# Optimization experiments

Hardware: AMD Instinct MI355X
Metric: run time of the kernel (lower is better)

## Reference

```python
import jax, jax.numpy as jnp
import numpy as np

D_MODEL = 512
NUM_HEADS = 8
D_K = D_MODEL // NUM_HEADS


def setup_inputs() -> dict:
    key = jax.random.key(0)
    k0, k1, k2, k3, k4 = jax.random.split(key, 5)
    s = 1.0 / np.sqrt(D_MODEL)
    return {
        "x": jax.random.normal(k0, (2, 4096, D_MODEL), dtype=jnp.float32),
        "W_q": jax.random.normal(k1, (D_MODEL, D_MODEL), dtype=jnp.float32) * s,
        "W_k": jax.random.normal(k2, (D_MODEL, D_MODEL), dtype=jnp.float32) * s,
        "W_v": jax.random.normal(k3, (D_MODEL, D_MODEL), dtype=jnp.float32) * s,
        "W_o": jax.random.normal(k4, (D_MODEL, D_MODEL), dtype=jnp.float32) * s,
    }


def reference(x, W_q, W_k, W_v, W_o):
    B, S, _ = x.shape
    # project and split heads: (B, H, S, d_k)
    def split(t):
        return t.reshape(B, S, NUM_HEADS, D_K).transpose(0, 2, 1, 3)
    Q = split(x @ W_q)
    K = split(x @ W_k)
    V = split(x @ W_v)
    scale = jnp.sqrt(jnp.asarray(D_K, dtype=x.dtype))
    logits = jnp.einsum('bhqd,bhkd->bhqk', Q, K) / scale
    attn = jax.nn.softmax(logits, axis=-1)  # dropout is identity at inference
    out = jnp.einsum('bhqk,bhkd->bhqd', attn, V)
    concat = out.transpose(0, 2, 1, 3).reshape(B, S, D_MODEL)
    return concat @ W_o
```

## Files before the change

### kernel.cpp

```cpp
#include <hip/hip_runtime.h>
#include <hip/hip_bf16.h>


#define DMODEL 512
#define SEQ    4096
#define NTOK   8192
#define LDQK   1024

using f32x4 = __attribute__((ext_vector_type(4))) float;
using s16x8 = __attribute__((ext_vector_type(8))) short;
using u16x8 = __attribute__((ext_vector_type(8))) unsigned short;

static __device__ __forceinline__ unsigned short f2bf(float f) {
  union { float f; unsigned u; } v; v.f = f;
  unsigned r = v.u + 0x7fff + ((v.u >> 16) & 1);
  return (unsigned short)(r >> 16);
}

static __device__ __forceinline__ unsigned pack_bf2(float lo, float hi) {
  __hip_bfloat162 t = __float22bfloat162_rn(make_float2(lo, hi));
  union { __hip_bfloat162 b; unsigned u; } c; c.b = t; return c.u;
}

static __device__ __forceinline__ void gll16(const void* g, void* l) {
  __builtin_amdgcn_global_load_lds(
      (const __attribute__((address_space(1))) unsigned int*)g,
      (__attribute__((address_space(3))) unsigned int*)l, 16, 0, 0);
}

__global__ void prep_kernel(const float* __restrict__ x,
                            const float* __restrict__ Wq,
                            const float* __restrict__ Wk,
                            const float* __restrict__ Wv,
                            const float* __restrict__ Wo,
                            unsigned short* __restrict__ xb,
                            unsigned short* __restrict__ Wall, float c2) {
  __shared__ float T[64][65];
  const int bx = blockIdx.x;
  if (bx < 1024) {
    for (int i = bx * 256 + threadIdx.x; i < NTOK * DMODEL / 4; i += 262144) {
      float4 v = ((const float4*)x)[i];
      ushort4 o;
      o.x = f2bf(v.x); o.y = f2bf(v.y); o.z = f2bf(v.z); o.w = f2bf(v.w);
      ((ushort4*)xb)[i] = o;
    }
    return;
  }
  const int t = bx - 1024;
  const int y = t >> 6, sub = t & 63;
  const float* W = (y == 0) ? Wq : (y == 1) ? Wk : (y == 2) ? Wv : Wo;
  const float scale = (y == 0) ? c2 : 1.0f;
  const int tk = (sub & 7) * 64;
  const int tn = (sub >> 3) * 64;
  const int r  = threadIdx.x >> 2;
  const int cq = threadIdx.x & 3;
#pragma unroll
  for (int i = 0; i < 4; ++i) {
    int c = (cq + 4 * i) * 4;
    float4 v = *(const float4*)&W[(size_t)(tk + r) * 512 + tn + c];
    T[r][c + 0] = v.x * scale; T[r][c + 1] = v.y * scale;
    T[r][c + 2] = v.z * scale; T[r][c + 3] = v.w * scale;
  }
  __syncthreads();
  const int n  = threadIdx.x >> 2;
  const int k0 = (threadIdx.x & 3) * 16;
#pragma unroll
  for (int j4 = 0; j4 < 4; ++j4) {
    ushort4 o;
    o.x = f2bf(T[k0 + j4 * 4 + 0][n]);
    o.y = f2bf(T[k0 + j4 * 4 + 1][n]);
    o.z = f2bf(T[k0 + j4 * 4 + 2][n]);
    o.w = f2bf(T[k0 + j4 * 4 + 3][n]);
    *(ushort4*)&Wall[(size_t)y * 262144 + (size_t)(tn + n) * 512 + tk + k0 + j4 * 4] = o;
  }
}

__global__ __launch_bounds__(256, 3) void gemm_qkv(
    const unsigned short* __restrict__ xb,
    const unsigned short* __restrict__ Wall,
    unsigned short* __restrict__ QKb,
    unsigned short* __restrict__ Vtb)
{
  __shared__ unsigned short As[128 * 64];
  __shared__ unsigned short Bs[128 * 64];
  const int by = blockIdx.y;
  const bool vmode = (by >= 8);
  const unsigned short* A  = vmode ? (Wall + 2 * 262144) : xb;
  const unsigned short* Bt = vmode ? xb : Wall;
  const size_t bm = vmode ? (size_t)(by - 8) * 128 : (size_t)blockIdx.x * 128;
  const size_t bn = vmode ? (size_t)blockIdx.x * 128 : (size_t)by * 128;
  const int tid  = threadIdx.x;
  const int wave = tid >> 6, lane = tid & 63;
  const int q4 = lane >> 4, ln = lane & 15;
  const int wm = (wave >> 1) * 64, wn = (wave & 1) * 64;
  f32x4 acc[4][4] = {};

  const int rlo  = lane >> 3;
  const int sbx  = ((lane & 7) << 4) ^ (rlo << 4);
  const int rswz = (ln & 7) << 4;

  const char* Asb = (const char*)A  + (size_t)(bm + wave * 32 + rlo) * 1024 + sbx;
  const char* Bsb = (const char*)Bt + (size_t)(bn + wave * 32 + rlo) * 1024 + sbx;
  char* Adst = (char*)As + wave * 4096;
  char* Bdst = (char*)Bs + wave * 4096;

  for (int kt = 0; kt < 512; kt += 64) {
    __syncthreads();
#pragma unroll
    for (int j = 0; j < 4; ++j) {
      gll16(Asb + kt * 2 + j * 8192, Adst + j * 1024);
      gll16(Bsb + kt * 2 + j * 8192, Bdst + j * 1024);
    }
    __syncthreads();
    s16x8 bfr[4][2];
#pragma unroll
    for (int ni = 0; ni < 4; ni++) {
      const char* bb = (char*)Bs + (wn + ni * 16 + ln) * 128;
      bfr[ni][0] = *(const s16x8*)(bb + ((q4 * 16)      ^ rswz));
      bfr[ni][1] = *(const s16x8*)(bb + ((q4 * 16 + 64) ^ rswz));
    }
#pragma unroll
    for (int mi = 0; mi < 4; mi++) {
      const char* ab = (char*)As + (wm + mi * 16 + ln) * 128;
      s16x8 af0 = *(const s16x8*)(ab + ((q4 * 16)      ^ rswz));
      s16x8 af1 = *(const s16x8*)(ab + ((q4 * 16 + 64) ^ rswz));
#pragma unroll
      for (int ni = 0; ni < 4; ni++) {
        acc[mi][ni] = __builtin_amdgcn_mfma_f32_16x16x32_bf16(
            af0, bfr[ni][0], acc[mi][ni], 0, 0, 0);
        acc[mi][ni] = __builtin_amdgcn_mfma_f32_16x16x32_bf16(
            af1, bfr[ni][1], acc[mi][ni], 0, 0, 0);
      }
    }
  }
#pragma unroll
  for (int mi = 0; mi < 4; mi++)
#pragma unroll
    for (int r = 0; r < 4; ++r) {
      size_t row = bm + wm + mi * 16 + q4 * 4 + r;
#pragma unroll
      for (int ni = 0; ni < 4; ni++) {
        size_t col = bn + wn + ni * 16 + ln;
        unsigned short hv = f2bf(acc[mi][ni][r]);
        if (!vmode) {
          QKb[row * 1024 + col] = hv;
        } else {
          int b = (int)(col >> 12), s = (int)(col & 4095);
          int sp = (s & ~63) | (s & 32) | (((s >> 2) & 3) << 3) |
                   (((s >> 4) & 1) << 2) | (s & 3);
          Vtb[(size_t)b * 2097152 + row * 4096 + sp] = hv;
        }
      }
    }
}

__global__ __launch_bounds__(256, 2) void attn_kernel(
    const unsigned short* __restrict__ QK,
    const unsigned short* __restrict__ Vt,
    unsigned short* __restrict__ Oc)
{
  const int bid = blockIdx.x + 32 * (blockIdx.y + 8 * blockIdx.z);
  const int lin = (bid & 7) * 64 + (bid >> 3);
  const int qt = lin & 31, bh = lin >> 5;
  const int h = bh & 7, b = bh >> 3;
  const int tid = threadIdx.x, wave = tid >> 6, lane = tid & 63;
  const int q4 = lane >> 4, ln = lane & 15;
  __shared__ unsigned short Ks[2][64 * 64];
  __shared__ unsigned short Vs[2][64 * 64];
  const size_t rowbase = (size_t)b * SEQ;
  const size_t qrow0   = (size_t)qt * 128 + wave * 32;
  const unsigned short* Kp  = QK + rowbase * LDQK + 512 + h * 64;
  const unsigned short* VTp = Vt + ((size_t)(b * 8 + h) * 64) * SEQ;

  s16x8 qf[2][2];
#pragma unroll
  for (int mf = 0; mf < 2; ++mf) {
    const unsigned short* q = QK + (rowbase + qrow0 + mf * 16 + ln) * LDQK + h * 64;
    qf[mf][0] = *(const s16x8*)(q + q4 * 8);
    qf[mf][1] = *(const s16x8*)(q + 32 + q4 * 8);
  }
  f32x4 o[2][4] = {};
  float lp[2] = {};

  const int srow = tid >> 2;
  const int c32  = (tid & 3) * 32;
  const int swz  = (srow & 7) << 4;
  const int wof0 = srow * 128 + ((c32 +  0) ^ swz);
  const int wof1 = srow * 128 + ((c32 + 16) ^ swz);
  const int rswz = (ln & 7) << 4;

  const unsigned short* kgp = Kp  + (size_t)srow * LDQK + (c32 >> 1);
  const unsigned short* vgp = VTp + (size_t)srow * SEQ + (c32 >> 1);

  u16x8 kr  = *(const u16x8*)kgp;
  u16x8 kr2 = *(const u16x8*)(kgp + 8);
  u16x8 vr  = *(const u16x8*)vgp;
  u16x8 vr2 = *(const u16x8*)(vgp + 8);
  *(u16x8*)((char*)Ks[0] + wof0) = kr;
  *(u16x8*)((char*)Ks[0] + wof1) = kr2;
  *(u16x8*)((char*)Vs[0] + wof0) = vr;
  *(u16x8*)((char*)Vs[0] + wof1) = vr2;
  kgp += (size_t)64 * LDQK;  vgp += 64;
  kr  = *(const u16x8*)kgp;
  kr2 = *(const u16x8*)(kgp + 8);
  vr  = *(const u16x8*)vgp;
  vr2 = *(const u16x8*)(vgp + 8);
  __syncthreads();

  const f32x4 fz = {0.f, 0.f, 0.f, 0.f};

  s16x8 vfp[2][4];
  s16x8 pfp[2][2];

  {
    const char* Kc = (const char*)Ks[0];
    const char* Vc = (const char*)Vs[0];
    f32x4 s4[2][4];
#pragma unroll
    for (int ni = 0; ni < 4; ni++) {
      const char* kb = Kc + (ni * 16 + ln) * 128;
      s16x8 kf0 = *(const s16x8*)(kb + ((q4 * 16)      ^ rswz));
      s16x8 kf1 = *(const s16x8*)(kb + ((q4 * 16 + 64) ^ rswz));
      __builtin_amdgcn_s_setprio(1);
#pragma unroll
      for (int mf = 0; mf < 2; ++mf) {
        f32x4 acc0 = __builtin_amdgcn_mfma_f32_16x16x32_bf16(kf0, qf[mf][0], fz, 0, 0, 0);
        s4[mf][ni] = __builtin_amdgcn_mfma_f32_16x16x32_bf16(kf1, qf[mf][1], acc0, 0, 0, 0);
      }
      __builtin_amdgcn_s_setprio(0);
    }
#pragma unroll
    for (int ks = 0; ks < 2; ++ks)
#pragma unroll
      for (int ni = 0; ni < 4; ni++)
        vfp[ks][ni] = *(const s16x8*)(Vc + (ni * 16 + ln) * 128 +
                                      ((ks * 64 + q4 * 16) ^ rswz));
#pragma unroll
    for (int mf = 0; mf < 2; ++mf) {
      float e[4][4];
#pragma unroll
      for (int ni = 0; ni < 4; ni++)
#pragma unroll
        for (int r = 0; r < 4; ++r)
          e[ni][r] = __builtin_amdgcn_exp2f(s4[mf][ni][r]);
      float t0 = (e[0][0] + e[0][1]) + (e[0][2] + e[0][3]);
      float t1 = (e[1][0] + e[1][1]) + (e[1][2] + e[1][3]);
      float t2 = (e[2][0] + e[2][1]) + (e[2][2] + e[2][3]);
      float t3 = (e[3][0] + e[3][1]) + (e[3][2] + e[3][3]);
      lp[mf] += (t0 + t1) + (t2 + t3);
#pragma unroll
      for (int ks = 0; ks < 2; ++ks) {
        union { s16x8 v; unsigned u[4]; } pu;
        pu.u[0] = pack_bf2(e[2 * ks][0],     e[2 * ks][1]);
        pu.u[1] = pack_bf2(e[2 * ks][2],     e[2 * ks][3]);
        pu.u[2] = pack_bf2(e[2 * ks + 1][0], e[2 * ks + 1][1]);
        pu.u[3] = pack_bf2(e[2 * ks + 1][2], e[2 * ks + 1][3]);
        pfp[mf][ks] = pu.v;
      }
    }
    char* Kn = (char*)Ks[1];
    char* Vn = (char*)Vs[1];
    *(u16x8*)(Kn + wof0) = kr;
    *(u16x8*)(Kn + wof1) = kr2;
    *(u16x8*)(Vn + wof0) = vr;
    *(u16x8*)(Vn + wof1) = vr2;
    kgp += (size_t)64 * LDQK;  vgp += 64;
    kr  = *(const u16x8*)kgp;
    kr2 = *(const u16x8*)(kgp + 8);
    vr  = *(const u16x8*)vgp;
    vr2 = *(const u16x8*)(vgp + 8);
    __syncthreads();
  }

#pragma unroll 2
  for (int t = 1; t < 64; ++t) {
    const int cur = t & 1;
    const char* Kc = (const char*)Ks[cur];
    const char* Vc = (const char*)Vs[cur];

    f32x4 s4[2][4];
#pragma unroll
    for (int ni = 0; ni < 4; ni++) {
      const char* kb = Kc + (ni * 16 + ln) * 128;
      s16x8 kf0 = *(const s16x8*)(kb + ((q4 * 16)      ^ rswz));
      s16x8 kf1 = *(const s16x8*)(kb + ((q4 * 16 + 64) ^ rswz));
      __builtin_amdgcn_s_setprio(1);
#pragma unroll
      for (int mf = 0; mf < 2; ++mf) {
        f32x4 acc0 = __builtin_amdgcn_mfma_f32_16x16x32_bf16(kf0, qf[mf][0], fz, 0, 0, 0);
        s4[mf][ni] = __builtin_amdgcn_mfma_f32_16x16x32_bf16(kf1, qf[mf][1], acc0, 0, 0, 0);
      }
      __builtin_amdgcn_s_setprio(0);
    }

#pragma unroll
    for (int ks = 0; ks < 2; ++ks)
#pragma unroll
      for (int ni = 0; ni < 4; ni++)
#pragma unroll
        for (int mf = 0; mf < 2; ++mf)
          o[mf][ni] = __builtin_amdgcn_mfma_f32_16x16x32_bf16(pfp[mf][ks], vfp[ks][ni], o[mf][ni], 0, 0, 0);

    s16x8 vfc[2][4];
#pragma unroll
    for (int ks = 0; ks < 2; ++ks)
#pragma unroll
      for (int ni = 0; ni < 4; ni++)
        vfc[ks][ni] = *(const s16x8*)(Vc + (ni * 16 + ln) * 128 +
                                      ((ks * 64 + q4 * 16) ^ rswz));

    s16x8 pfc[2][2];
#pragma unroll
    for (int mf = 0; mf < 2; ++mf) {
      float e[4][4];
#pragma unroll
      for (int ni = 0; ni < 4; ni++)
#pragma unroll
        for (int r = 0; r < 4; ++r)
          e[ni][r] = __builtin_amdgcn_exp2f(s4[mf][ni][r]);
      float t0 = (e[0][0] + e[0][1]) + (e[0][2] + e[0][3]);
      float t1 = (e[1][0] + e[1][1]) + (e[1][2] + e[1][3]);
      float t2 = (e[2][0] + e[2][1]) + (e[2][2] + e[2][3]);
      float t3 = (e[3][0] + e[3][1]) + (e[3][2] + e[3][3]);
      lp[mf] += (t0 + t1) + (t2 + t3);
#pragma unroll
      for (int ks = 0; ks < 2; ++ks) {
        union { s16x8 v; unsigned u[4]; } pu;
        pu.u[0] = pack_bf2(e[2 * ks][0],     e[2 * ks][1]);
        pu.u[1] = pack_bf2(e[2 * ks][2],     e[2 * ks][3]);
        pu.u[2] = pack_bf2(e[2 * ks + 1][0], e[2 * ks + 1][1]);
        pu.u[3] = pack_bf2(e[2 * ks + 1][2], e[2 * ks + 1][3]);
        pfc[mf][ks] = pu.v;
      }
    }

    if (t + 1 < 64) {
      char* Kn = (char*)Ks[cur ^ 1];
      char* Vn = (char*)Vs[cur ^ 1];
      *(u16x8*)(Kn + wof0) = kr;
      *(u16x8*)(Kn + wof1) = kr2;
      *(u16x8*)(Vn + wof0) = vr;
      *(u16x8*)(Vn + wof1) = vr2;
      if (t + 2 < 64) {
        kgp += (size_t)64 * LDQK;  vgp += 64;
        kr  = *(const u16x8*)kgp;
        kr2 = *(const u16x8*)(kgp + 8);
        vr  = *(const u16x8*)vgp;
        vr2 = *(const u16x8*)(vgp + 8);
      }
    }

#pragma unroll
    for (int ks = 0; ks < 2; ++ks)
#pragma unroll
      for (int ni = 0; ni < 4; ni++)
        vfp[ks][ni] = vfc[ks][ni];
#pragma unroll
    for (int mf = 0; mf < 2; ++mf)
#pragma unroll
      for (int ks = 0; ks < 2; ++ks)
        pfp[mf][ks] = pfc[mf][ks];

    __syncthreads();
  }

  __builtin_amdgcn_s_setprio(1);
#pragma unroll
  for (int ks = 0; ks < 2; ++ks)
#pragma unroll
    for (int ni = 0; ni < 4; ni++)
#pragma unroll
      for (int mf = 0; mf < 2; ++mf)
        o[mf][ni] = __builtin_amdgcn_mfma_f32_16x16x32_bf16(pfp[mf][ks], vfp[ks][ni], o[mf][ni], 0, 0, 0);
  __builtin_amdgcn_s_setprio(0);

#pragma unroll
  for (int mf = 0; mf < 2; ++mf) {
    float l = lp[mf];
    l += __shfl_xor(l, 16, 64);
    l += __shfl_xor(l, 32, 64);
    const float inv = 1.0f / l;
#pragma unroll
    for (int r = 0; r < 4; ++r) {
      const float nv = __shfl(inv, q4 * 4 + r, 64);
      const size_t row = rowbase + qrow0 + mf * 16 + q4 * 4 + r;
#pragma unroll
      for (int ni = 0; ni < 4; ni++)
        Oc[row * 512 + h * 64 + ni * 16 + ln] = f2bf(o[mf][ni][r] * nv);
    }
  }
}

__global__ __launch_bounds__(256, 3) void gemm_out(
    const unsigned short* __restrict__ A,
    const unsigned short* __restrict__ Bt,
    float* __restrict__ C)
{
  __shared__ unsigned short As[128 * 64];
  __shared__ unsigned short Bs[64 * 64];
  const int tid  = threadIdx.x;
  const int wave = tid >> 6, lane = tid & 63;
  const int q4 = lane >> 4, ln = lane & 15;
  const size_t bm = (size_t)blockIdx.x * 128;
  const size_t bn = (size_t)blockIdx.y * 64;
  const int wm = (wave >> 1) * 64, wn = (wave & 1) * 32;
  f32x4 acc[4][2] = {};

  const int rlo  = lane >> 3;
  const int sbx  = ((lane & 7) << 4) ^ (rlo << 4);
  const int rswz = (ln & 7) << 4;

  const char* Asb = (const char*)A  + (size_t)(bm + wave * 32 + rlo) * 1024 + sbx;
  const char* Bsb = (const char*)Bt + (size_t)(bn + wave * 16 + rlo) * 1024 + sbx;
  char* Adst = (char*)As + wave * 4096;
  char* Bdst = (char*)Bs + wave * 2048;

  for (int kt = 0; kt < 512; kt += 64) {
    __syncthreads();
#pragma unroll
    for (int j = 0; j < 4; ++j)
      gll16(Asb + kt * 2 + j * 8192, Adst + j * 1024);
#pragma unroll
    for (int j = 0; j < 2; ++j)
      gll16(Bsb + kt * 2 + j * 8192, Bdst + j * 1024);
    __syncthreads();
    s16x8 bfr[2][2];
#pragma unroll
    for (int ni = 0; ni < 2; ni++) {
      const char* bb = (char*)Bs + (wn + ni * 16 + ln) * 128;
      bfr[ni][0] = *(const s16x8*)(bb + ((q4 * 16)      ^ rswz));
      bfr[ni][1] = *(const s16x8*)(bb + ((q4 * 16 + 64) ^ rswz));
    }
#pragma unroll
    for (int mi = 0; mi < 4; mi++) {
      const char* ab = (char*)As + (wm + mi * 16 + ln) * 128;
      s16x8 af0 = *(const s16x8*)(ab + ((q4 * 16)      ^ rswz));
      s16x8 af1 = *(const s16x8*)(ab + ((q4 * 16 + 64) ^ rswz));
#pragma unroll
      for (int ni = 0; ni < 2; ni++) {
        acc[mi][ni] = __builtin_amdgcn_mfma_f32_16x16x32_bf16(
            af0, bfr[ni][0], acc[mi][ni], 0, 0, 0);
        acc[mi][ni] = __builtin_amdgcn_mfma_f32_16x16x32_bf16(
            af1, bfr[ni][1], acc[mi][ni], 0, 0, 0);
      }
    }
  }
#pragma unroll
  for (int mi = 0; mi < 4; mi++)
#pragma unroll
    for (int r = 0; r < 4; ++r) {
      size_t row = bm + wm + mi * 16 + q4 * 4 + r;
#pragma unroll
      for (int ni = 0; ni < 2; ni++)
        C[row * 512 + bn + wn + ni * 16 + ln] = acc[mi][ni][r];
    }
}

extern "C" void kernel_launch(void* const* d_in, const int* in_sizes, int n_in,
                              void* d_out, int out_size, void* d_ws, size_t ws_size,
                              hipStream_t stream) {
  const float* x  = (const float*)d_in[0];
  const float* Wq = (const float*)d_in[1];
  const float* Wk = (const float*)d_in[2];
  const float* Wv = (const float*)d_in[3];
  const float* Wo = (const float*)d_in[4];

  char* ws = (char*)d_ws;
  unsigned short* xb    = (unsigned short*)(ws);
  unsigned short* Wall  = (unsigned short*)(ws + 8388608);
  unsigned short* QKb   = (unsigned short*)(ws + 10485760);
  unsigned short* Vtb   = (unsigned short*)(ws + 27262976);
  unsigned short* Oc    = (unsigned short*)(ws + 35651584);

  const float C2 = 0.125f * 1.44269504088896f;

  hipLaunchKernelGGL(prep_kernel, dim3(1280), dim3(256), 0, stream,
                     x, Wq, Wk, Wv, Wo, xb, Wall, C2);
  hipLaunchKernelGGL(gemm_qkv, dim3(64, 12), dim3(256), 0, stream,
                     xb, Wall, QKb, Vtb);
  hipLaunchKernelGGL(attn_kernel, dim3(32, 8, 2), dim3(256), 0, stream,
                     QKb, Vtb, Oc);
  hipLaunchKernelGGL(gemm_out, dim3(64, 8), dim3(256), 0, stream,
                     Oc, Wall + 3 * 262144, (float*)d_out);
}
```

Baseline: 181.7 us.

## Use direct global-to-LDS async loads and smaller 128-thread attention blocks

The attention kernel's K/V staging changes from register-buffered loads followed by LDS stores to direct global-to-LDS loads (gll16), issued one tile ahead at the start of each iteration. Blocks shrink from 4 waves over 128 query rows to 2 waves over 64 rows, which doubles the grid. The aim is to remove the VGPR staging and explicit LDS writes and to get more blocks for occupancy. The cost is that each block now reads K/V for only half as many queries, so global traffic per query roughly doubles.

```diff
diff --git a/kernel.cpp b/kernel.cpp
--- a/kernel.cpp
+++ b/kernel.cpp
@@ -154,21 +154,21 @@
     }
 }
 
-__global__ __launch_bounds__(256, 2) void attn_kernel(
+__global__ __launch_bounds__(128, 2) void attn_kernel(
     const unsigned short* __restrict__ QK,
     const unsigned short* __restrict__ Vt,
     unsigned short* __restrict__ Oc)
 {
-  const int bid = blockIdx.x + 32 * (blockIdx.y + 8 * blockIdx.z);
-  const int lin = (bid & 7) * 64 + (bid >> 3);
-  const int qt = lin & 31, bh = lin >> 5;
+  const int bid = blockIdx.x + 64 * (blockIdx.y + 8 * blockIdx.z);
+  const int lin = (bid & 7) * 128 + (bid >> 3);
+  const int qt = lin & 63, bh = lin >> 6;
   const int h = bh & 7, b = bh >> 3;
   const int tid = threadIdx.x, wave = tid >> 6, lane = tid & 63;
   const int q4 = lane >> 4, ln = lane & 15;
   __shared__ unsigned short Ks[2][64 * 64];
   __shared__ unsigned short Vs[2][64 * 64];
   const size_t rowbase = (size_t)b * SEQ;
-  const size_t qrow0   = (size_t)qt * 128 + wave * 32;
+  const size_t qrow0   = (size_t)qt * 64 + wave * 32;
   const unsigned short* Kp  = QK + rowbase * LDQK + 512 + h * 64;
   const unsigned short* VTp = Vt + ((size_t)(b * 8 + h) * 64) * SEQ;
 
@@ -182,29 +182,26 @@
   f32x4 o[2][4] = {};
   float lp[2] = {};
 
-  const int srow = tid >> 2;
-  const int c32  = (tid & 3) * 32;
-  const int swz  = (srow & 7) << 4;
-  const int wof0 = srow * 128 + ((c32 +  0) ^ swz);
-  const int wof1 = srow * 128 + ((c32 + 16) ^ swz);
   const int rswz = (ln & 7) << 4;
 
-  const unsigned short* kgp = Kp  + (size_t)srow * LDQK + (c32 >> 1);
-  const unsigned short* vgp = VTp + (size_t)srow * SEQ + (c32 >> 1);
-
-  u16x8 kr  = *(const u16x8*)kgp;
-  u16x8 kr2 = *(const u16x8*)(kgp + 8);
-  u16x8 vr  = *(const u16x8*)vgp;
-  u16x8 vr2 = *(const u16x8*)(vgp + 8);
-  *(u16x8*)((char*)Ks[0] + wof0) = kr;
-  *(u16x8*)((char*)Ks[0] + wof1) = kr2;
-  *(u16x8*)((char*)Vs[0] + wof0) = vr;
-  *(u16x8*)((char*)Vs[0] + wof1) = vr2;
-  kgp += (size_t)64 * LDQK;  vgp += 64;
-  kr  = *(const u16x8*)kgp;
-  kr2 = *(const u16x8*)(kgp + 8);
-  vr  = *(const u16x8*)vgp;
-  vr2 = *(const u16x8*)(vgp + 8);
+  const int rlo = lane >> 3;
+  const int sb  = ((lane & 7) << 4) ^ (rlo << 4);
+  const char* kgb = (const char*)Kp  + (size_t)(wave * 32 + rlo) * 2048 + sb;
+  const char* vgb = (const char*)VTp + (size_t)(wave * 32 + rlo) * 8192 + sb;
+
+  auto stage = [&](int tt, int nb) {
+    char* Kd = (char*)Ks[nb] + wave * 4096;
+    char* Vd = (char*)Vs[nb] + wave * 4096;
+    const char* kg = kgb + (size_t)tt * 131072;
+    const char* vg = vgb + (size_t)tt * 128;
+#pragma unroll
+    for (int j = 0; j < 4; ++j) {
+      gll16(kg + j * 16384, Kd + j * 1024);
+      gll16(vg + (size_t)j * 65536, Vd + j * 1024);
+    }
+  };
+
+  stage(0, 0);
   __syncthreads();
 
   const f32x4 fz = {0.f, 0.f, 0.f, 0.f};
@@ -215,6 +212,7 @@
   {
     const char* Kc = (const char*)Ks[0];
     const char* Vc = (const char*)Vs[0];
+    stage(1, 1);
     f32x4 s4[2][4];
 #pragma unroll
     for (int ni = 0; ni < 4; ni++) {
@@ -258,17 +256,6 @@
         pfp[mf][ks] = pu.v;
       }
     }
-    char* Kn = (char*)Ks[1];
-    char* Vn = (char*)Vs[1];
-    *(u16x8*)(Kn + wof0) = kr;
-    *(u16x8*)(Kn + wof1) = kr2;
-    *(u16x8*)(Vn + wof0) = vr;
-    *(u16x8*)(Vn + wof1) = vr2;
-    kgp += (size_t)64 * LDQK;  vgp += 64;
-    kr  = *(const u16x8*)kgp;
-    kr2 = *(const u16x8*)(kgp + 8);
-    vr  = *(const u16x8*)vgp;
-    vr2 = *(const u16x8*)(vgp + 8);
     __syncthreads();
   }
 
@@ -277,6 +264,8 @@
     const int cur = t & 1;
     const char* Kc = (const char*)Ks[cur];
     const char* Vc = (const char*)Vs[cur];
+
+    if (t + 1 < 64) stage(t + 1, cur ^ 1);
 
     f32x4 s4[2][4];
 #pragma unroll
@@ -331,22 +320,6 @@
         pu.u[2] = pack_bf2(e[2 * ks + 1][0], e[2 * ks + 1][1]);
         pu.u[3] = pack_bf2(e[2 * ks + 1][2], e[2 * ks + 1][3]);
         pfc[mf][ks] = pu.v;
-      }
-    }
-
-    if (t + 1 < 64) {
-      char* Kn = (char*)Ks[cur ^ 1];
-      char* Vn = (char*)Vs[cur ^ 1];
-      *(u16x8*)(Kn + wof0) = kr;
-      *(u16x8*)(Kn + wof1) = kr2;
-      *(u16x8*)(Vn + wof0) = vr;
-      *(u16x8*)(Vn + wof1) = vr2;
-      if (t + 2 < 64) {
-        kgp += (size_t)64 * LDQK;  vgp += 64;
-        kr  = *(const u16x8*)kgp;
-        kr2 = *(const u16x8*)(kgp + 8);
-        vr  = *(const u16x8*)vgp;
-        vr2 = *(const u16x8*)(vgp + 8);
       }
     }
 
@@ -478,7 +451,7 @@
                      x, Wq, Wk, Wv, Wo, xb, Wall, C2);
   hipLaunchKernelGGL(gemm_qkv, dim3(64, 12), dim3(256), 0, stream,
                      xb, Wall, QKb, Vtb);
-  hipLaunchKernelGGL(attn_kernel, dim3(32, 8, 2), dim3(256), 0, stream,
+  hipLaunchKernelGGL(attn_kernel, dim3(64, 8, 2), dim3(128), 0, stream,
                      QKb, Vtb, Oc);
   hipLaunchKernelGGL(gemm_out, dim3(64, 8), dim3(256), 0, stream,
                      Oc, Wall + 3 * 262144, (float*)d_out);
```

Result: slower. 202.3 us (+11.3%).
